# Performance work log

Measured on AMD Instinct MI355X. Metric: run time of the kernel, lower is better.

The kernel has to match this reference:

```python
import jax, jax.numpy as jnp
import numpy as np

D_MODEL = 1024
N_HEAD = 16
SEQ = 2048
BATCH = 2


def setup_inputs() -> dict:
    key = jax.random.key(0)
    x = jax.random.normal(key, (BATCH, SEQ, D_MODEL), dtype=jnp.float32)
    return {"x": x}


def reference(x) -> jnp.ndarray:
    B, S, D = x.shape
    H = N_HEAD
    hd = D // H
    # split heads: q=k=v=x -> [B, H, S, hd]
    qkv = x.reshape(B, S, H, hd).transpose(0, 2, 1, 3)
    q = k = v = qkv
    # scores [B, H, S, S], scaled by sqrt(head_dim)
    w = jnp.einsum("bhqd,bhkd->bhqk", q, k) / jnp.sqrt(jnp.asarray(hd, x.dtype))
    # causal mask (nd == ns == S here)
    causal = jnp.tril(jnp.ones((S, S), dtype=bool))
    mask_value = jnp.finfo(w.dtype).min
    w = jnp.where(causal[None, None, :, :], w, mask_value)
    w = jax.nn.softmax(w, axis=-1)
    out = jnp.einsum("bhqk,bhkd->bhqd", w, v)
    # merge heads -> [B, S, D]
    return out.transpose(0, 2, 1, 3).reshape(B, S, D)
```

## Files before the change

kernel.cpp:

```cpp
#include <hip/hip_runtime.h>
#include <hip/hip_bf16.h>

#define BATCH  2
#define SEQ    2048
#define DMODEL 1024
#define NHEAD  16
#define HD     64
#define BH     (BATCH * NHEAD)

typedef __attribute__((ext_vector_type(8))) short s8v;
typedef __attribute__((ext_vector_type(4))) float f4v;

#define QK_BETA 0.42466089f

__device__ inline unsigned short bf16_rne(float f) {
    unsigned u = __builtin_bit_cast(unsigned, f);
    u += 0x7FFFu + ((u >> 16) & 1u);
    return (unsigned short)(u >> 16);
}

__device__ __forceinline__ unsigned pk_bf16(float lo, float hi) {
    __hip_bfloat162 h = __float22bfloat162_rn(make_float2(lo, hi));
    unsigned u;
    __builtin_memcpy(&u, &h, 4);
    return u;
}

__global__ __launch_bounds__(256) void prep_kernel(const float* __restrict__ x,
                                                   unsigned short* __restrict__ xb,
                                                   unsigned short* __restrict__ xbT) {
    __shared__ unsigned short tileT[64 * 40];
    const int id = blockIdx.x;
    const int bh = id & (BH - 1);
    const int st = id >> 5;
    const int b = bh >> 4, h = bh & (NHEAD - 1);
    const int s0 = st * 32;
    const int tid = threadIdx.x;
    const int c4 = tid & 15, r16 = tid >> 4;

    const size_t off0 = (size_t)(b * SEQ + s0 + r16) * DMODEL + h * HD + c4 * 4;
    const size_t off1 = (size_t)(b * SEQ + s0 + 16 + r16) * DMODEL + h * HD + c4 * 4;
    const float4 v0 = *(const float4*)(x + off0);
    const float4 v1 = *(const float4*)(x + off1);

    {
        uint2 u;
        u.x = pk_bf16(v0.x * QK_BETA, v0.y * QK_BETA);
        u.y = pk_bf16(v0.z * QK_BETA, v0.w * QK_BETA);
        *(uint2*)(xb + off0) = u;
        u.x = pk_bf16(v1.x * QK_BETA, v1.y * QK_BETA);
        u.y = pk_bf16(v1.z * QK_BETA, v1.w * QK_BETA);
        *(uint2*)(xb + off1) = u;
    }
    {
        const int d0 = c4 * 4;
        unsigned short* t0 = tileT + r16;
        t0[(d0 + 0) * 40] = bf16_rne(v0.x);
        t0[(d0 + 1) * 40] = bf16_rne(v0.y);
        t0[(d0 + 2) * 40] = bf16_rne(v0.z);
        t0[(d0 + 3) * 40] = bf16_rne(v0.w);
        unsigned short* t1 = tileT + 16 + r16;
        t1[(d0 + 0) * 40] = bf16_rne(v1.x);
        t1[(d0 + 1) * 40] = bf16_rne(v1.y);
        t1[(d0 + 2) * 40] = bf16_rne(v1.z);
        t1[(d0 + 3) * 40] = bf16_rne(v1.w);
    }
    __syncthreads();
    {
        const int d = tid >> 2;
        const int sq = (tid & 3) * 8;
        const s8v o = *(const s8v*)(tileT + d * 40 + sq);
        *(s8v*)(xbT + (size_t)(bh * HD + d) * SEQ + s0 + sq) = o;
    }
}

__device__ __forceinline__ void stage_tile(const unsigned short* __restrict__ xbh,
                                           const unsigned short* __restrict__ xTh,
                                           char* lds, int bufoff, int k0,
                                           int w, int sr, int sc) {
    if (w < 2) {
#pragma unroll
        for (int i = 0; i < 4; ++i) {
            const int r = w * 32 + i * 8 + sr;
            const unsigned short* gsrc =
                xbh + (size_t)(k0 + r) * DMODEL + ((sc ^ (r & 7)) * 8);
            const int loff = __builtin_amdgcn_readfirstlane(bufoff + (w * 32 + i * 8) * 128);
            __builtin_amdgcn_global_load_lds(
                (const __attribute__((address_space(1))) void*)gsrc,
                (__attribute__((address_space(3))) void*)(lds + loff), 16, 0, 0);
        }
    } else {
#pragma unroll
        for (int i = 0; i < 4; ++i) {
            const int d = (w - 2) * 32 + i * 8 + sr;
            const unsigned short* gsrc =
                xTh + (size_t)d * SEQ + k0 + ((sc ^ (d & 7)) * 8);
            const int loff =
                __builtin_amdgcn_readfirstlane(bufoff + 8192 + ((w - 2) * 32 + i * 8) * 128);
            __builtin_amdgcn_global_load_lds(
                (const __attribute__((address_space(1))) void*)gsrc,
                (__attribute__((address_space(3))) void*)(lds + loff), 16, 0, 0);
        }
    }
}

__global__ __launch_bounds__(256, 4) void flash_kernel(const unsigned short* __restrict__ xb,
                                                       const unsigned short* __restrict__ xbT,
                                                       float* __restrict__ out) {
    __shared__ __align__(16) char lds[40960];

    const int id = blockIdx.x;
    const int bh = id & (BH - 1);
    const int t5 = id >> 5;
    const int rr = t5 >> 3, uu = t5 & 7;
    const int qt = (rr == 0) ? (31 - uu) : (rr == 1) ? (16 + uu)
                 : (rr == 2) ? (15 - uu) : uu;
    const int b = bh >> 4, h = bh & (NHEAD - 1);
    const int tid = threadIdx.x;
    const int w = tid >> 6;
    const int lane = tid & 63;
    const int n = lane & 15;
    const int g = lane >> 4;
    const int qbase = qt * 64;

    const unsigned short* xbh = xb + (size_t)b * SEQ * DMODEL + h * HD;
    const unsigned short* xTh = xbT + (size_t)bh * HD * SEQ;

    const int qrow = qbase + w * 16 + n;
    const s8v qf0 = *(const s8v*)(xbh + (size_t)qrow * DMODEL + g * 8);
    const s8v qf1 = *(const s8v*)(xbh + (size_t)qrow * DMODEL + 32 + g * 8);

    s8v ones;
#pragma unroll
    for (int j = 0; j < 8; ++j) ones[j] = (short)0x3F80;

    int roff0[4], roff1[4];
#pragma unroll
    for (int t = 0; t < 4; ++t) {
        roff0[t] = (t * 16 + n) * 128 + ((g ^ (n & 7)) * 16);
        roff1[t] = (t * 16 + n) * 128 + (((4 + g) ^ (n & 7)) * 16);
    }

    f4v o0 = {0.f, 0.f, 0.f, 0.f}, o1 = o0, o2 = o0, o3 = o0;
    f4v lacc = o0;
    char* const Pbase = lds + 32768 + w * 2048;

    char* wrP[4];
#pragma unroll
    for (int t = 0; t < 4; ++t)
        wrP[t] = Pbase + (t >> 1) * 1024 + n * 64 +
                 ((((t & 1) * 2 + (g >> 1)) ^ (n & 3)) * 16) + (g & 1) * 8;
    const char* rdP = Pbase + n * 64 + ((g ^ (n & 3)) * 16);

    const int sr = lane >> 3;
    const int sc = lane & 7;

    stage_tile(xbh, xTh, lds, 0, 0, w, sr, sc);

    for (int kt = 0; kt <= qt; ++kt) {
        char* const buf = lds + ((kt & 1) << 14);
        __syncthreads();
        if (kt < qt)
            stage_tile(xbh, xTh, lds, ((kt & 1) ^ 1) << 14, (kt + 1) * 64, w, sr, sc);

        const bool diag = (kt == qt);
#pragma unroll
        for (int t = 0; t < 4; ++t) {
            const s8v kb0 = *(const s8v*)(buf + roff0[t]);
            const s8v kb1 = *(const s8v*)(buf + roff1[t]);
            f4v c = {0.f, 0.f, 0.f, 0.f};
            __builtin_amdgcn_s_setprio(1);
            c = __builtin_amdgcn_mfma_f32_16x16x32_bf16(kb0, qf0, c, 0, 0, 0);
            c = __builtin_amdgcn_mfma_f32_16x16x32_bf16(kb1, qf1, c, 0, 0, 0);
            __builtin_amdgcn_s_setprio(0);
            float p0 = __builtin_amdgcn_exp2f(c[0]);
            float p1 = __builtin_amdgcn_exp2f(c[1]);
            float p2 = __builtin_amdgcn_exp2f(c[2]);
            float p3 = __builtin_amdgcn_exp2f(c[3]);
            if (diag) {
                const int kl = t * 16 + g * 4, ql = w * 16 + n;
                p0 = (kl + 0 <= ql) ? p0 : 0.0f;
                p1 = (kl + 1 <= ql) ? p1 : 0.0f;
                p2 = (kl + 2 <= ql) ? p2 : 0.0f;
                p3 = (kl + 3 <= ql) ? p3 : 0.0f;
            }
            uint2 u;
            u.x = pk_bf16(p0, p1);
            u.y = pk_bf16(p2, p3);
            *(uint2*)(wrP[t]) = u;
        }

        const s8v pa0 = *(const s8v*)(rdP);
        const s8v pa1 = *(const s8v*)(rdP + 1024);
        const char* kColB = buf + 8192;
        {
            s8v vb;
            __builtin_amdgcn_s_setprio(1);
            lacc = __builtin_amdgcn_mfma_f32_16x16x32_bf16(pa0, ones, lacc, 0, 0, 0);
            vb = *(const s8v*)(kColB + roff0[0]);
            o0 = __builtin_amdgcn_mfma_f32_16x16x32_bf16(pa0, vb, o0, 0, 0, 0);
            vb = *(const s8v*)(kColB + roff1[0]);
            o0 = __builtin_amdgcn_mfma_f32_16x16x32_bf16(pa1, vb, o0, 0, 0, 0);
            vb = *(const s8v*)(kColB + roff0[1]);
            o1 = __builtin_amdgcn_mfma_f32_16x16x32_bf16(pa0, vb, o1, 0, 0, 0);
            vb = *(const s8v*)(kColB + roff1[1]);
            o1 = __builtin_amdgcn_mfma_f32_16x16x32_bf16(pa1, vb, o1, 0, 0, 0);
            lacc = __builtin_amdgcn_mfma_f32_16x16x32_bf16(pa1, ones, lacc, 0, 0, 0);
            vb = *(const s8v*)(kColB + roff0[2]);
            o2 = __builtin_amdgcn_mfma_f32_16x16x32_bf16(pa0, vb, o2, 0, 0, 0);
            vb = *(const s8v*)(kColB + roff1[2]);
            o2 = __builtin_amdgcn_mfma_f32_16x16x32_bf16(pa1, vb, o2, 0, 0, 0);
            vb = *(const s8v*)(kColB + roff0[3]);
            o3 = __builtin_amdgcn_mfma_f32_16x16x32_bf16(pa0, vb, o3, 0, 0, 0);
            vb = *(const s8v*)(kColB + roff1[3]);
            o3 = __builtin_amdgcn_mfma_f32_16x16x32_bf16(pa1, vb, o3, 0, 0, 0);
            __builtin_amdgcn_s_setprio(0);
        }
    }

    f4v inv;
#pragma unroll
    for (int r = 0; r < 4; ++r)
        inv[r] = 1.0f / lacc[r];

    float* outh = out + (size_t)b * SEQ * DMODEL + h * HD;
#pragma unroll
    for (int r = 0; r < 4; ++r) {
        const size_t rowoff = (size_t)(qbase + w * 16 + g * 4 + r) * DMODEL;
        outh[rowoff + 0 * 16 + n] = o0[r] * inv[r];
        outh[rowoff + 1 * 16 + n] = o1[r] * inv[r];
        outh[rowoff + 2 * 16 + n] = o2[r] * inv[r];
        outh[rowoff + 3 * 16 + n] = o3[r] * inv[r];
    }
}

#define KT 32
#define QR 16
#define LDS_STRIDE 68

__global__ __launch_bounds__(64, 2)
void attn_fp32_kernel(const float* __restrict__ x, float* __restrict__ out) {
    __shared__ float kv[KT * LDS_STRIDE];
    const int id = blockIdx.x;
    const int bh = id & (BATCH * NHEAD - 1);
    const int qt = (SEQ / QR - 1) - (id >> 5);
    const int b = bh >> 4, h = bh & (NHEAD - 1);
    const int lane = threadIdx.x;
    const int row = lane & (QR - 1);
    const int slice = lane >> 4;
    const int qrow = qt * QR + row;
    const float* xh = x + (size_t)b * SEQ * DMODEL + (size_t)h * HD;
    float q[HD], o[HD];
    const float4* qp = (const float4*)(xh + (size_t)qrow * DMODEL);
#pragma unroll
    for (int i = 0; i < HD / 4; ++i) {
        float4 v = qp[i];
        q[4*i+0] = v.x * 0.125f; q[4*i+1] = v.y * 0.125f;
        q[4*i+2] = v.z * 0.125f; q[4*i+3] = v.w * 0.125f;
    }
#pragma unroll
    for (int d = 0; d < HD; ++d) o[d] = 0.0f;
    float l = 0.0f;
    const int kend = qt * QR + QR;
    for (int kt0 = 0; kt0 < kend; kt0 += KT) {
        __syncthreads();
#pragma unroll
        for (int i = 0; i < (KT * HD / 4) / 64; ++i) {
            int idx = i * 64 + lane;
            int r = idx >> 4, cc = idx & 15;
            *(float4*)(kv + r * LDS_STRIDE + cc * 4) =
                *(const float4*)(xh + (size_t)(kt0 + r) * DMODEL + cc * 4);
        }
        __syncthreads();
#pragma unroll 2
        for (int jj = 0; jj < KT / 4; ++jj) {
            const int j = jj * 4 + slice;
            const float* kr = kv + j * LDS_STRIDE;
            float a0 = 0.f, a1 = 0.f, a2 = 0.f, a3 = 0.f;
#pragma unroll
            for (int dq = 0; dq < 16; ++dq) {
                float4 kk = ((const float4*)kr)[dq];
                a0 = fmaf(q[4*dq+0], kk.x, a0); a1 = fmaf(q[4*dq+1], kk.y, a1);
                a2 = fmaf(q[4*dq+2], kk.z, a2); a3 = fmaf(q[4*dq+3], kk.w, a3);
            }
            float p = __expf((a0 + a1) + (a2 + a3));
            p = (kt0 + j <= qrow) ? p : 0.0f;
            l += p;
#pragma unroll
            for (int dq = 0; dq < 16; ++dq) {
                float4 vv = ((const float4*)kr)[dq];
                o[4*dq+0] = fmaf(p, vv.x, o[4*dq+0]); o[4*dq+1] = fmaf(p, vv.y, o[4*dq+1]);
                o[4*dq+2] = fmaf(p, vv.z, o[4*dq+2]); o[4*dq+3] = fmaf(p, vv.w, o[4*dq+3]);
            }
        }
    }
    l += __shfl_xor(l, 16, 64);
    l += __shfl_xor(l, 32, 64);
#pragma unroll
    for (int d = 0; d < HD; ++d) {
        o[d] += __shfl_xor(o[d], 16, 64);
        o[d] += __shfl_xor(o[d], 32, 64);
    }
    if (slice == 0) {
        const float invl = 1.0f / l;
        float4* op = (float4*)(out + ((size_t)b * SEQ + qrow) * DMODEL + (size_t)h * HD);
#pragma unroll
        for (int i = 0; i < HD / 4; ++i) {
            float4 v;
            v.x = o[4*i+0] * invl; v.y = o[4*i+1] * invl;
            v.z = o[4*i+2] * invl; v.w = o[4*i+3] * invl;
            op[i] = v;
        }
    }
}

extern "C" void kernel_launch(void* const* d_in, const int* in_sizes, int n_in,
                              void* d_out, int out_size, void* d_ws, size_t ws_size,
                              hipStream_t stream) {
    const float* x = (const float*)d_in[0];
    float* out = (float*)d_out;
    const size_t nXb = (size_t)BATCH * SEQ * DMODEL;
    const size_t need = 2 * nXb * 2;
    if (ws_size >= need) {
        unsigned short* xb  = (unsigned short*)d_ws;
        unsigned short* xbT = xb + nXb;
        hipLaunchKernelGGL(prep_kernel, dim3(BH * SEQ / 32), dim3(256), 0, stream,
                           x, xb, xbT);
        hipLaunchKernelGGL(flash_kernel, dim3(BH * SEQ / 64), dim3(256), 0, stream,
                           xb, xbT, out);
    } else {
        hipLaunchKernelGGL(attn_fp32_kernel, dim3(BATCH * NHEAD * (SEQ / QR)), dim3(64), 0,
                           stream, x, out);
    }
}
```

Before: 103.7 us.

## Switch flash kernel to 32x32 MFMA with 128-row query tiles

Rewrites the bf16 flash attention kernel so each block covers 128 query rows (32 per wave) and uses 32x32x16 MFMA instructions instead of 16x16x32. Each staged K/V tile is now reused by twice as many query rows, and the row sum is accumulated in VALU rather than with a ones-MFMA. Waves whose rows are fully masked skip their tile, and masking is applied only near the diagonal. The price is larger accumulators, more LDS, lower occupancy (2 blocks per CU) and half as many blocks, with the query-tile order simplified.

```diff
diff --git a/kernel.cpp b/kernel.cpp
--- a/kernel.cpp
+++ b/kernel.cpp
@@ -9,7 +9,7 @@
 #define BH     (BATCH * NHEAD)
 
 typedef __attribute__((ext_vector_type(8))) short s8v;
-typedef __attribute__((ext_vector_type(4))) float f4v;
+typedef __attribute__((ext_vector_type(16))) float f16v;
 
 #define QK_BETA 0.42466089f
 
@@ -104,133 +104,143 @@
     }
 }
 
-__global__ __launch_bounds__(256, 4) void flash_kernel(const unsigned short* __restrict__ xb,
+__global__ __launch_bounds__(256, 2) void flash_kernel(const unsigned short* __restrict__ xb,
                                                        const unsigned short* __restrict__ xbT,
                                                        float* __restrict__ out) {
-    __shared__ __align__(16) char lds[40960];
+    __shared__ __align__(16) char lds[49152];
 
     const int id = blockIdx.x;
     const int bh = id & (BH - 1);
-    const int t5 = id >> 5;
-    const int rr = t5 >> 3, uu = t5 & 7;
-    const int qt = (rr == 0) ? (31 - uu) : (rr == 1) ? (16 + uu)
-                 : (rr == 2) ? (15 - uu) : uu;
+    const int j = id >> 5;
+    const int qt = (j < 8) ? (15 - j) : (j - 8);
     const int b = bh >> 4, h = bh & (NHEAD - 1);
     const int tid = threadIdx.x;
     const int w = tid >> 6;
     const int lane = tid & 63;
-    const int n = lane & 15;
-    const int g = lane >> 4;
-    const int qbase = qt * 64;
+    const int qh = lane & 31;
+    const int hh = lane >> 5;
+    const int qbase = qt * 128;
 
     const unsigned short* xbh = xb + (size_t)b * SEQ * DMODEL + h * HD;
     const unsigned short* xTh = xbT + (size_t)bh * HD * SEQ;
 
-    const int qrow = qbase + w * 16 + n;
-    const s8v qf0 = *(const s8v*)(xbh + (size_t)qrow * DMODEL + g * 8);
-    const s8v qf1 = *(const s8v*)(xbh + (size_t)qrow * DMODEL + 32 + g * 8);
-
-    s8v ones;
-#pragma unroll
-    for (int j = 0; j < 8; ++j) ones[j] = (short)0x3F80;
-
-    int roff0[4], roff1[4];
-#pragma unroll
-    for (int t = 0; t < 4; ++t) {
-        roff0[t] = (t * 16 + n) * 128 + ((g ^ (n & 7)) * 16);
-        roff1[t] = (t * 16 + n) * 128 + (((4 + g) ^ (n & 7)) * 16);
-    }
-
-    f4v o0 = {0.f, 0.f, 0.f, 0.f}, o1 = o0, o2 = o0, o3 = o0;
-    f4v lacc = o0;
-    char* const Pbase = lds + 32768 + w * 2048;
-
-    char* wrP[4];
-#pragma unroll
-    for (int t = 0; t < 4; ++t)
-        wrP[t] = Pbase + (t >> 1) * 1024 + n * 64 +
-                 ((((t & 1) * 2 + (g >> 1)) ^ (n & 3)) * 16) + (g & 1) * 8;
-    const char* rdP = Pbase + n * 64 + ((g ^ (n & 3)) * 16);
+    const int qrow = qbase + w * 32 + qh;
+    s8v qf0 = *(const s8v*)(xbh + (size_t)qrow * DMODEL + 0 * 16 + hh * 8);
+    s8v qf1 = *(const s8v*)(xbh + (size_t)qrow * DMODEL + 1 * 16 + hh * 8);
+    s8v qf2 = *(const s8v*)(xbh + (size_t)qrow * DMODEL + 2 * 16 + hh * 8);
+    s8v qf3 = *(const s8v*)(xbh + (size_t)qrow * DMODEL + 3 * 16 + hh * 8);
+
+    int kbo[2][4];
+    int vbo[2][4];
+#pragma unroll
+    for (int i2 = 0; i2 < 2; ++i2)
+#pragma unroll
+        for (int c = 0; c < 4; ++c) {
+            kbo[i2][c] = (i2 * 32 + qh) * 128 + (((2 * c + hh) ^ (qh & 7)) * 16);
+            vbo[i2][c] = 8192 + (i2 * 32 + qh) * 128 + (((2 * c + hh) ^ (qh & 7)) * 16);
+        }
+
+    char* const Pbase = lds + 32768 + w * 4096;
+    int pwo0[4], pwo1[4], pro[4];
+#pragma unroll
+    for (int j2 = 0; j2 < 4; ++j2) {
+        pwo0[j2] = qh * 128 + (((j2 + 0) ^ (qh & 7)) * 16) + 8 * hh;
+        pwo1[j2] = qh * 128 + (((j2 + 4) ^ (qh & 7)) * 16) + 8 * hh;
+        pro[j2]  = qh * 128 + (((2 * j2 + hh) ^ (qh & 7)) * 16);
+    }
+
+    f16v o0 = {0,0,0,0,0,0,0,0,0,0,0,0,0,0,0,0};
+    f16v o1 = o0;
+    float lsum = 0.0f;
 
     const int sr = lane >> 3;
     const int sc = lane & 7;
 
     stage_tile(xbh, xTh, lds, 0, 0, w, sr, sc);
 
-    for (int kt = 0; kt <= qt; ++kt) {
+    const int ktEnd = 2 * qt + 1;
+    for (int kt = 0; kt <= ktEnd; ++kt) {
         char* const buf = lds + ((kt & 1) << 14);
         __syncthreads();
-        if (kt < qt)
+        if (kt < ktEnd)
             stage_tile(xbh, xTh, lds, ((kt & 1) ^ 1) << 14, (kt + 1) * 64, w, sr, sc);
 
-        const bool diag = (kt == qt);
-#pragma unroll
-        for (int t = 0; t < 4; ++t) {
-            const s8v kb0 = *(const s8v*)(buf + roff0[t]);
-            const s8v kb1 = *(const s8v*)(buf + roff1[t]);
-            f4v c = {0.f, 0.f, 0.f, 0.f};
-            __builtin_amdgcn_s_setprio(1);
-            c = __builtin_amdgcn_mfma_f32_16x16x32_bf16(kb0, qf0, c, 0, 0, 0);
-            c = __builtin_amdgcn_mfma_f32_16x16x32_bf16(kb1, qf1, c, 0, 0, 0);
-            __builtin_amdgcn_s_setprio(0);
-            float p0 = __builtin_amdgcn_exp2f(c[0]);
-            float p1 = __builtin_amdgcn_exp2f(c[1]);
-            float p2 = __builtin_amdgcn_exp2f(c[2]);
-            float p3 = __builtin_amdgcn_exp2f(c[3]);
-            if (diag) {
-                const int kl = t * 16 + g * 4, ql = w * 16 + n;
-                p0 = (kl + 0 <= ql) ? p0 : 0.0f;
-                p1 = (kl + 1 <= ql) ? p1 : 0.0f;
-                p2 = (kl + 2 <= ql) ? p2 : 0.0f;
-                p3 = (kl + 3 <= ql) ? p3 : 0.0f;
+        const int base_off = qbase + w * 32 - kt * 64;
+        if (base_off + 31 < 0) continue;
+        const bool fullLive = (base_off >= 63);
+        const int qlim = base_off + qh;
+
+        f16v c0 = {0,0,0,0,0,0,0,0,0,0,0,0,0,0,0,0};
+        f16v c1 = c0;
+        __builtin_amdgcn_s_setprio(1);
+        c0 = __builtin_amdgcn_mfma_f32_32x32x16_bf16(*(const s8v*)(buf + kbo[0][0]), qf0, c0, 0, 0, 0);
+        c0 = __builtin_amdgcn_mfma_f32_32x32x16_bf16(*(const s8v*)(buf + kbo[0][1]), qf1, c0, 0, 0, 0);
+        c0 = __builtin_amdgcn_mfma_f32_32x32x16_bf16(*(const s8v*)(buf + kbo[0][2]), qf2, c0, 0, 0, 0);
+        c0 = __builtin_amdgcn_mfma_f32_32x32x16_bf16(*(const s8v*)(buf + kbo[0][3]), qf3, c0, 0, 0, 0);
+        c1 = __builtin_amdgcn_mfma_f32_32x32x16_bf16(*(const s8v*)(buf + kbo[1][0]), qf0, c1, 0, 0, 0);
+        c1 = __builtin_amdgcn_mfma_f32_32x32x16_bf16(*(const s8v*)(buf + kbo[1][1]), qf1, c1, 0, 0, 0);
+        c1 = __builtin_amdgcn_mfma_f32_32x32x16_bf16(*(const s8v*)(buf + kbo[1][2]), qf2, c1, 0, 0, 0);
+        c1 = __builtin_amdgcn_mfma_f32_32x32x16_bf16(*(const s8v*)(buf + kbo[1][3]), qf3, c1, 0, 0, 0);
+        __builtin_amdgcn_s_setprio(0);
+
+        float p0[16], p1[16];
+#pragma unroll
+        for (int e = 0; e < 16; ++e) {
+            p0[e] = __builtin_amdgcn_exp2f(c0[e]);
+            p1[e] = __builtin_amdgcn_exp2f(c1[e]);
+        }
+        if (!fullLive) {
+#pragma unroll
+            for (int e = 0; e < 16; ++e) {
+                const int kl = (e & 3) + 8 * (e >> 2) + 4 * hh;
+                p0[e] = (kl <= qlim) ? p0[e] : 0.0f;
+                p1[e] = (kl + 32 <= qlim) ? p1[e] : 0.0f;
             }
+        }
+#pragma unroll
+        for (int e = 0; e < 16; ++e) lsum += p0[e] + p1[e];
+#pragma unroll
+        for (int j2 = 0; j2 < 4; ++j2) {
             uint2 u;
-            u.x = pk_bf16(p0, p1);
-            u.y = pk_bf16(p2, p3);
-            *(uint2*)(wrP[t]) = u;
-        }
-
-        const s8v pa0 = *(const s8v*)(rdP);
-        const s8v pa1 = *(const s8v*)(rdP + 1024);
-        const char* kColB = buf + 8192;
-        {
-            s8v vb;
-            __builtin_amdgcn_s_setprio(1);
-            lacc = __builtin_amdgcn_mfma_f32_16x16x32_bf16(pa0, ones, lacc, 0, 0, 0);
-            vb = *(const s8v*)(kColB + roff0[0]);
-            o0 = __builtin_amdgcn_mfma_f32_16x16x32_bf16(pa0, vb, o0, 0, 0, 0);
-            vb = *(const s8v*)(kColB + roff1[0]);
-            o0 = __builtin_amdgcn_mfma_f32_16x16x32_bf16(pa1, vb, o0, 0, 0, 0);
-            vb = *(const s8v*)(kColB + roff0[1]);
-            o1 = __builtin_amdgcn_mfma_f32_16x16x32_bf16(pa0, vb, o1, 0, 0, 0);
-            vb = *(const s8v*)(kColB + roff1[1]);
-            o1 = __builtin_amdgcn_mfma_f32_16x16x32_bf16(pa1, vb, o1, 0, 0, 0);
-            lacc = __builtin_amdgcn_mfma_f32_16x16x32_bf16(pa1, ones, lacc, 0, 0, 0);
-            vb = *(const s8v*)(kColB + roff0[2]);
-            o2 = __builtin_amdgcn_mfma_f32_16x16x32_bf16(pa0, vb, o2, 0, 0, 0);
-            vb = *(const s8v*)(kColB + roff1[2]);
-            o2 = __builtin_amdgcn_mfma_f32_16x16x32_bf16(pa1, vb, o2, 0, 0, 0);
-            vb = *(const s8v*)(kColB + roff0[3]);
-            o3 = __builtin_amdgcn_mfma_f32_16x16x32_bf16(pa0, vb, o3, 0, 0, 0);
-            vb = *(const s8v*)(kColB + roff1[3]);
-            o3 = __builtin_amdgcn_mfma_f32_16x16x32_bf16(pa1, vb, o3, 0, 0, 0);
-            __builtin_amdgcn_s_setprio(0);
-        }
-    }
-
-    f4v inv;
-#pragma unroll
-    for (int r = 0; r < 4; ++r)
-        inv[r] = 1.0f / lacc[r];
+            u.x = pk_bf16(p0[4 * j2 + 0], p0[4 * j2 + 1]);
+            u.y = pk_bf16(p0[4 * j2 + 2], p0[4 * j2 + 3]);
+            *(uint2*)(Pbase + pwo0[j2]) = u;
+            u.x = pk_bf16(p1[4 * j2 + 0], p1[4 * j2 + 1]);
+            u.y = pk_bf16(p1[4 * j2 + 2], p1[4 * j2 + 3]);
+            *(uint2*)(Pbase + pwo1[j2]) = u;
+        }
+
+        const s8v pa0 = *(const s8v*)(Pbase + pro[0]);
+        const s8v pa1 = *(const s8v*)(Pbase + pro[1]);
+        const s8v pa2 = *(const s8v*)(Pbase + pro[2]);
+        const s8v pa3 = *(const s8v*)(Pbase + pro[3]);
+        __builtin_amdgcn_s_setprio(1);
+        o0 = __builtin_amdgcn_mfma_f32_32x32x16_bf16(pa0, *(const s8v*)(buf + vbo[0][0]), o0, 0, 0, 0);
+        o1 = __builtin_amdgcn_mfma_f32_32x32x16_bf16(pa0, *(const s8v*)(buf + vbo[1][0]), o1, 0, 0, 0);
+        o0 = __builtin_amdgcn_mfma_f32_32x32x16_bf16(pa1, *(const s8v*)(buf + vbo[0][1]), o0, 0, 0, 0);
+        o1 = __builtin_amdgcn_mfma_f32_32x32x16_bf16(pa1, *(const s8v*)(buf + vbo[1][1]), o1, 0, 0, 0);
+        o0 = __builtin_amdgcn_mfma_f32_32x32x16_bf16(pa2, *(const s8v*)(buf + vbo[0][2]), o0, 0, 0, 0);
+        o1 = __builtin_amdgcn_mfma_f32_32x32x16_bf16(pa2, *(const s8v*)(buf + vbo[1][2]), o1, 0, 0, 0);
+        o0 = __builtin_amdgcn_mfma_f32_32x32x16_bf16(pa3, *(const s8v*)(buf + vbo[0][3]), o0, 0, 0, 0);
+        o1 = __builtin_amdgcn_mfma_f32_32x32x16_bf16(pa3, *(const s8v*)(buf + vbo[1][3]), o1, 0, 0, 0);
+        __builtin_amdgcn_s_setprio(0);
+    }
+
+    lsum += __shfl_xor(lsum, 32, 64);
+    float invr[16];
+#pragma unroll
+    for (int e = 0; e < 16; ++e) {
+        const int rowq = (e & 3) + 8 * (e >> 2) + 4 * hh;
+        invr[e] = 1.0f / __shfl(lsum, rowq, 64);
+    }
 
     float* outh = out + (size_t)b * SEQ * DMODEL + h * HD;
 #pragma unroll
-    for (int r = 0; r < 4; ++r) {
-        const size_t rowoff = (size_t)(qbase + w * 16 + g * 4 + r) * DMODEL;
-        outh[rowoff + 0 * 16 + n] = o0[r] * inv[r];
-        outh[rowoff + 1 * 16 + n] = o1[r] * inv[r];
-        outh[rowoff + 2 * 16 + n] = o2[r] * inv[r];
-        outh[rowoff + 3 * 16 + n] = o3[r] * inv[r];
+    for (int e = 0; e < 16; ++e) {
+        const int rowq = (e & 3) + 8 * (e >> 2) + 4 * hh;
+        const size_t ro = (size_t)(qbase + w * 32 + rowq) * DMODEL;
+        outh[ro + 0 * 32 + qh] = o0[e] * invr[e];
+        outh[ro + 1 * 32 + qh] = o1[e] * invr[e];
     }
 }
 
@@ -326,7 +336,7 @@
         unsigned short* xbT = xb + nXb;
         hipLaunchKernelGGL(prep_kernel, dim3(BH * SEQ / 32), dim3(256), 0, stream,
                            x, xb, xbT);
-        hipLaunchKernelGGL(flash_kernel, dim3(BH * SEQ / 64), dim3(256), 0, stream,
+        hipLaunchKernelGGL(flash_kernel, dim3(BH * SEQ / 128), dim3(256), 0, stream,
                            xb, xbT, out);
     } else {
         hipLaunchKernelGGL(attn_fp32_kernel, dim3(BATCH * NHEAD * (SEQ / QR)), dim3(64), 0,
```

Result: slower. 106.5 us (+2.7%).
